# Performance work log

Hardware: AMD Instinct MI355X
Metric: run time of the kernel (lower is better)

## Reference

```python
import jax, jax.numpy as jnp
import numpy as np

GATE_THRESH = 0.4
ALPHA_FN = lambda L: 1.0 - 1.0 / L  # length-adaptive alpha, called with actual L
EPS_NORM = 1e-12  # F.normalize eps
EPS_LN = 1e-5     # LayerNorm eps


def setup_inputs() -> dict:
    key = jax.random.key(0)
    B, L, H, V = 64, 2048, 128, 32000
    ks = jax.random.split(key, 8)
    s = lambda k, shape, fan: jax.random.normal(k, shape, jnp.float32) * (1.0 / np.sqrt(fan))
    return {
        "seq": jax.random.randint(ks[0], (B, L), 0, V, dtype=jnp.int64),
        "embed_w": jax.random.normal(ks[1], (V, H), jnp.float32) * 0.02,
        "ff_w1": s(ks[2], (2 * H, H), H), "ff_b1": jnp.zeros((2 * H,), jnp.float32),
        "ff_w2": s(ks[3], (H, 2 * H), 2 * H), "ff_b2": jnp.zeros((H,), jnp.float32),
        "ln_g": jnp.ones((H,), jnp.float32), "ln_b": jnp.zeros((H,), jnp.float32),
        "kp_w": s(ks[4], (H, H), H),
        "rp_w": s(ks[5], (H, H), H), "rp_b": jnp.zeros((H,), jnp.float32),
        "out_w": s(ks[6], (V, H), H), "out_b": jnpp if False else jnp.zeros((V,), jnp.float32),
    }


def reference(seq, embed_w, ff_w1, ff_b1, ff_w2, ff_b2, ln_g, ln_b, kp_w, rp_w, rp_b, out_w, out_b):
    h = embed_w[seq]                                            # [B,L,H]
    ff = jnp.maximum(h @ ff_w1.T + ff_b1, 0.0) @ ff_w2.T + ff_b2
    x = h + ff
    mu = x.mean(-1, keepdims=True)
    var = x.var(-1, keepdims=True)                              # biased, as LayerNorm
    h = (x - mu) / jnp.sqrt(var + EPS_LN) * ln_g + ln_b
    B, L, H = h.shape
    alpha = ALPHA_FN(L)
    k_all = jnp.einsum('blh,oh->blo', h, kp_w)                  # kp has no bias

    def step(M, k):                                             # M:[B,H,H], k:[B,H]
        kn = k / jnp.maximum(jnp.linalg.norm(k, axis=-1, keepdims=True), EPS_NORM)
        vp = jnp.einsum('bij,bj->bi', M, kn)
        d = k - vp
        delta = d[:, :, None] * kn[:, None, :]                  # outer product [B,H,H]
        fire = (jnp.linalg.norm(d, axis=-1) >= GATE_THRESH * jnp.linalg.norm(k, axis=-1)).astype(k.dtype)
        return M + (1.0 - alpha) * fire[:, None, None] * delta, None

    M0 = jnp.zeros((B, H, H), h.dtype)
    M, _ = jax.lax.scan(step, M0, jnp.swapaxes(k_all[:, :-1, :], 0, 1))  # scan over L-1 steps
    q = k_all[:, -1, :]
    read = jnp.einsum('bij,bj->bi', M, q)
    return (read @ rp_w.T + rp_b) @ out_w.T + out_b             # [B,V]
```

## Files before the change

kernel.cpp:

```cpp
#include <hip/hip_runtime.h>
#include <hip/hip_bf16.h>
#include <stdint.h>

#define Bn 64
#define Ln 2048
#define Hn 128
#define Vn 32000
#define THn 256
#define LAMBDA_ (1.0f/2048.0f)
#define CC 32
#define NCH (Ln/CC)
#define KP  132
#define VS  132
#define VPW (CC*VS)
#define ADS 131
#define ADW (CC*ADS+4)
#define GS  36
#define GXS 33
#define MSR 36
#define MSW 576
#define HS  132

typedef short bf16x8 __attribute__((ext_vector_type(8)));
typedef float f32x4  __attribute__((ext_vector_type(4)));

__device__ __forceinline__ float rdlane(float v, int s) {
  return __int_as_float(__builtin_amdgcn_readlane(__float_as_int(v), s));
}

template <int CTRL>
__device__ __forceinline__ float dpp_add(float x) {
  int t = __builtin_amdgcn_update_dpp(0, __float_as_int(x), CTRL, 0xf, 0xf, false);
  return x + __int_as_float(t);
}
__device__ __forceinline__ float wave_sum64(float x) {
  x = dpp_add<0x111>(x);
  x = dpp_add<0x112>(x);
  x = dpp_add<0x114>(x);
  x = dpp_add<0x118>(x);
  x = dpp_add<0x142>(x);
  x = dpp_add<0x143>(x);
  return rdlane(x, 63);
}

__device__ __forceinline__ uint32_t packhl(float x) {
  uint32_t bx = __float_as_uint(x);
  float hf = __uint_as_float(bx & 0xFFFF0000u);
  uint32_t bl = __float_as_uint(x - hf);
  return (bx >> 16) | (bl & 0xFFFF0000u);
}
__device__ __forceinline__ float unpackhl(uint32_t u) {
  return __uint_as_float(u << 16) + __uint_as_float(u & 0xFFFF0000u);
}

struct FragHL { bf16x8 h; bf16x8 l; };
__device__ __forceinline__ FragHL mkfrag(const uint32_t* u) {
  union { uint32_t a[4]; bf16x8 v; } H, L;
  H.a[0] = __builtin_amdgcn_perm(u[1], u[0], 0x05040100u);
  H.a[1] = __builtin_amdgcn_perm(u[3], u[2], 0x05040100u);
  H.a[2] = __builtin_amdgcn_perm(u[5], u[4], 0x05040100u);
  H.a[3] = __builtin_amdgcn_perm(u[7], u[6], 0x05040100u);
  L.a[0] = __builtin_amdgcn_perm(u[1], u[0], 0x07060302u);
  L.a[1] = __builtin_amdgcn_perm(u[3], u[2], 0x07060302u);
  L.a[2] = __builtin_amdgcn_perm(u[5], u[4], 0x07060302u);
  L.a[3] = __builtin_amdgcn_perm(u[7], u[6], 0x07060302u);
  FragHL f; f.h = H.v; f.l = L.v; return f;
}

__device__ __forceinline__ void ld8(const uint32_t* p, uint32_t* u) {
  const uint4 a = *reinterpret_cast<const uint4*>(p);
  const uint4 b = *reinterpret_cast<const uint4*>(p + 4);
  u[0]=a.x; u[1]=a.y; u[2]=a.z; u[3]=a.w;
  u[4]=b.x; u[5]=b.y; u[6]=b.z; u[7]=b.w;
}

__device__ __forceinline__ bf16x8 asbf(uint4 u) {
  union { uint4 a; bf16x8 v; } c; c.a = u; return c.v;
}

__device__ __forceinline__ f32x4 mfma16(bf16x8 a, bf16x8 b, f32x4 c) {
  return __builtin_amdgcn_mfma_f32_16x16x32_bf16(a, b, c, 0, 0, 0);
}

__device__ __forceinline__ void gload_lds4(const uint32_t* g, uint32_t* l) {
  __builtin_amdgcn_global_load_lds(
      (const __attribute__((address_space(1))) void*)g,
      (__attribute__((address_space(3))) void*)l, 4, 0, 0);
}

__global__ __launch_bounds__(256) void p0_pack(
    const float* __restrict__ w1, const float* __restrict__ w2,
    const float* __restrict__ kp, uint32_t* __restrict__ wp)
{
  const int id = blockIdx.x*256 + threadIdx.x;
  const float* src; uint32_t *dh, *dl; int p;
  if (id < 16384)      { src = w1; p = id;         dh = wp;         dl = wp+16384; }
  else if (id < 32768) { src = w2; p = id-16384;   dh = wp+32768;   dl = wp+49152; }
  else                 { src = kp; p = id-32768;   dh = wp+65536;   dl = wp+73728; }
  const float x0 = src[2*p], x1 = src[2*p+1];
  const uint32_t b0 = __float_as_uint(x0), b1 = __float_as_uint(x1);
  const float l0f = x0 - __uint_as_float(b0 & 0xFFFF0000u);
  const float l1f = x1 - __uint_as_float(b1 & 0xFFFF0000u);
  dh[p] = (b0 >> 16) | ((b1 >> 16) << 16);
  dl[p] = (__float_as_uint(l0f) >> 16) | ((__float_as_uint(l1f) >> 16) << 16);
}

__global__ __launch_bounds__(256, 2) void p1_fused(
    const int* __restrict__ seq,
    const float* __restrict__ embed_w,
    const uint32_t* __restrict__ wp,
    const float* __restrict__ ff_b1, const float* __restrict__ ff_b2,
    const float* __restrict__ ln_g, const float* __restrict__ ln_b,
    uint32_t* __restrict__ knp_all, float* __restrict__ norm_all)
{
  __shared__ __align__(16) uint32_t h_p[64*HS];
  __shared__ __align__(16) uint32_t u_p[64*HS];
  __shared__ float part1[256], part2[256];
  __shared__ float mul[64], rsl[64];
  __shared__ int sid[64];

  const int tid  = threadIdx.x;
  const int lane = tid & 63;
  const int w    = __builtin_amdgcn_readfirstlane(tid >> 6);
  const int q4   = lane >> 4;
  const int m16  = lane & 15;
  const int tile0 = blockIdx.x * 64;

  const uint32_t* w1h = wp;
  const uint32_t* w1l = wp + 16384;
  const uint32_t* w2h = wp + 32768;
  const uint32_t* w2l = wp + 49152;
  const uint32_t* kph = wp + 65536;
  const uint32_t* kpl = wp + 73728;

  if (tid < 64) sid[tid] = seq[tile0 + tid];
  __syncthreads();

  {
    const int t = tid >> 2, part = tid & 3;
    const float4* erow =
        reinterpret_cast<const float4*>(embed_w + (size_t)sid[t]*Hn) + part*8;
    #pragma unroll
    for (int c = 0; c < 8; ++c) {
      float4 v = erow[c];
      int j = part*32 + c*4;
      h_p[t*HS+j+0] = packhl(v.x); h_p[t*HS+j+1] = packhl(v.y);
      h_p[t*HS+j+2] = packhl(v.z); h_p[t*HS+j+3] = packhl(v.w);
    }
  }
  __syncthreads();

  f32x4 acc2[4][2];
  #pragma unroll
  for (int tt=0;tt<4;++tt)
    #pragma unroll
    for (int ct=0;ct<2;++ct) acc2[tt][ct] = (f32x4){0.f,0.f,0.f,0.f};

  #pragma unroll 1
  for (int ho=0; ho<2; ++ho) {
    #pragma unroll 1
    for (int tt=0; tt<4; ++tt) {
      FragHL fa[4];
      #pragma unroll
      for (int kk=0;kk<4;++kk) {
        uint32_t ua[8];
        ld8(&h_p[(16*tt+m16)*HS + 32*kk + 8*q4], ua);
        fa[kk] = mkfrag(ua);
      }
      #pragma unroll
      for (int ct=0; ct<2; ++ct) {
        const int ob = 128*ho + 32*w + 16*ct;
        f32x4 a = (f32x4){0.f,0.f,0.f,0.f};
        #pragma unroll
        for (int kk=0;kk<4;++kk) {
          const size_t wi = (size_t)(ob+m16)*64 + 16*kk + 4*q4;
          bf16x8 bh = asbf(*reinterpret_cast<const uint4*>(&w1h[wi]));
          bf16x8 bl = asbf(*reinterpret_cast<const uint4*>(&w1l[wi]));
          a = mfma16(fa[kk].h, bh, a);
          a = mfma16(fa[kk].h, bl, a);
          a = mfma16(fa[kk].l, bh, a);
        }
        const float bb = ff_b1[ob + m16];
        #pragma unroll
        for (int reg=0;reg<4;++reg) {
          float uv = fmaxf(a[reg] + bb, 0.f);
          u_p[(16*tt+4*q4+reg)*HS + 32*w + 16*ct + m16] = packhl(uv);
        }
      }
    }
    __syncthreads();
    #pragma unroll 1
    for (int tt=0; tt<4; ++tt) {
      FragHL fu[4];
      #pragma unroll
      for (int kk=0;kk<4;++kk) {
        uint32_t ua[8];
        ld8(&u_p[(16*tt+m16)*HS + 32*kk + 8*q4], ua);
        fu[kk] = mkfrag(ua);
      }
      #pragma unroll
      for (int ct=0; ct<2; ++ct) {
        const int ib = 32*w + 16*ct;
        f32x4 a = acc2[tt][ct];
        #pragma unroll
        for (int kk=0;kk<4;++kk) {
          const size_t wi = (size_t)(ib+m16)*128 + 64*ho + 16*kk + 4*q4;
          bf16x8 bh = asbf(*reinterpret_cast<const uint4*>(&w2h[wi]));
          bf16x8 bl = asbf(*reinterpret_cast<const uint4*>(&w2l[wi]));
          a = mfma16(fu[kk].h, bh, a);
          a = mfma16(fu[kk].h, bl, a);
          a = mfma16(fu[kk].l, bh, a);
        }
        acc2[tt][ct] = a;
      }
    }
    __syncthreads();
  }

  float xx[4][2][4];
  #pragma unroll
  for (int tt=0;tt<4;++tt)
    #pragma unroll
    for (int ct=0;ct<2;++ct) {
      const int col = 32*w + 16*ct + m16;
      const float b2 = ff_b2[col];
      #pragma unroll
      for (int reg=0;reg<4;++reg) {
        const float hval = unpackhl(h_p[(16*tt+4*q4+reg)*HS + col]);
        xx[tt][ct][reg] = acc2[tt][ct][reg] + b2 + hval;
      }
    }
  #pragma unroll
  for (int tt=0;tt<4;++tt)
    #pragma unroll
    for (int reg=0;reg<4;++reg) {
      float s1 = xx[tt][0][reg] + xx[tt][1][reg];
      float s2 = xx[tt][0][reg]*xx[tt][0][reg] + xx[tt][1][reg]*xx[tt][1][reg];
      s1 += __shfl_xor(s1,1); s1 += __shfl_xor(s1,2);
      s1 += __shfl_xor(s1,4); s1 += __shfl_xor(s1,8);
      s2 += __shfl_xor(s2,1); s2 += __shfl_xor(s2,2);
      s2 += __shfl_xor(s2,4); s2 += __shfl_xor(s2,8);
      if (m16==0) {
        part1[w*64 + 16*tt+4*q4+reg] = s1;
        part2[w*64 + 16*tt+4*q4+reg] = s2;
      }
    }
  __syncthreads();
  if (tid < 64) {
    const float mu = (part1[tid]+part1[64+tid]+part1[128+tid]+part1[192+tid])*(1.0f/128.0f);
    const float ms = (part2[tid]+part2[64+tid]+part2[128+tid]+part2[192+tid])*(1.0f/128.0f);
    mul[tid] = mu;
    rsl[tid] = rsqrtf(ms - mu*mu + 1e-5f);
  }
  __syncthreads();

  #pragma unroll
  for (int tt=0;tt<4;++tt)
    #pragma unroll
    for (int ct=0;ct<2;++ct) {
      const int col = 32*w + 16*ct + m16;
      const float g = ln_g[col], bb = ln_b[col];
      #pragma unroll
      for (int reg=0;reg<4;++reg) {
        const int tok = 16*tt+4*q4+reg;
        const float hn = (xx[tt][ct][reg] - mul[tok])*rsl[tok]*g + bb;
        h_p[tok*HS + col] = packhl(hn);
      }
    }
  __syncthreads();

  f32x4 ak[4][2];
  #pragma unroll 1
  for (int tt=0;tt<4;++tt) {
    FragHL fh[4];
    #pragma unroll
    for (int kk=0;kk<4;++kk) {
      uint32_t ua[8];
      ld8(&h_p[(16*tt+m16)*HS + 32*kk + 8*q4], ua);
      fh[kk] = mkfrag(ua);
    }
    #pragma unroll
    for (int ct=0;ct<2;++ct) {
      const int ob = 32*w + 16*ct;
      f32x4 a = (f32x4){0.f,0.f,0.f,0.f};
      #pragma unroll
      for (int kk=0;kk<4;++kk) {
        const size_t wi = (size_t)(ob+m16)*64 + 16*kk + 4*q4;
        bf16x8 bh = asbf(*reinterpret_cast<const uint4*>(&kph[wi]));
        bf16x8 bl = asbf(*reinterpret_cast<const uint4*>(&kpl[wi]));
        a = mfma16(fh[kk].h, bh, a);
        a = mfma16(fh[kk].h, bl, a);
        a = mfma16(fh[kk].l, bh, a);
      }
      ak[tt][ct] = a;
    }
  }
  #pragma unroll
  for (int tt=0;tt<4;++tt)
    #pragma unroll
    for (int reg=0;reg<4;++reg) {
      float s = ak[tt][0][reg]*ak[tt][0][reg] + ak[tt][1][reg]*ak[tt][1][reg];
      s += __shfl_xor(s,1); s += __shfl_xor(s,2);
      s += __shfl_xor(s,4); s += __shfl_xor(s,8);
      if (m16==0) part1[w*64 + 16*tt+4*q4+reg] = s;
    }
  __syncthreads();
  if (tid < 64) {
    const float nn = part1[tid]+part1[64+tid]+part1[128+tid]+part1[192+tid];
    const float nrm = sqrtf(nn);
    norm_all[tile0 + tid] = nrm;
    mul[tid] = 1.0f / fmaxf(nrm, 1e-12f);
  }
  __syncthreads();
  #pragma unroll
  for (int tt=0;tt<4;++tt)
    #pragma unroll
    for (int ct=0;ct<2;++ct) {
      const int col = 32*w + 16*ct + m16;
      #pragma unroll
      for (int reg=0;reg<4;++reg) {
        const int tok = 16*tt+4*q4+reg;
        knp_all[(size_t)(tile0+tok)*Hn + col] = packhl(ak[tt][ct][reg]*mul[tok]);
      }
    }
}

__global__ __launch_bounds__(576, 1) void p2_scan(
    const uint32_t* __restrict__ knp_all, const float* __restrict__ norm_all,
    float* __restrict__ read_ws)
{
  const int tid  = threadIdx.x;
  const int lane = tid & 63;
  const int wv   = __builtin_amdgcn_readfirstlane(tid >> 6);
  const int q    = lane >> 4;
  const int m    = lane & 15;
  const int b    = blockIdx.x;

  __shared__ __align__(16) uint32_t kn_p[3*CC*KP];
  __shared__ __align__(16) float    vp0L[2*VPW];
  __shared__ __align__(16) float    adL [2*ADW];
  __shared__ __align__(16) float    Gt  [2*CC*GS];
  __shared__ __align__(16) float    GxT [CC*GXS];
  __shared__ __align__(16) uint32_t msc [8*MSW];
  __shared__ float nrm_l[3*CC];

  f32x4 Macc[8];
  #pragma unroll
  for (int ct=0; ct<8; ++ct) Macc[ct] = (f32x4){0.f,0.f,0.f,0.f};

  const uint32_t* knb = knp_all + (size_t)b*Ln*Hn;
  const float*    nb  = norm_all + (size_t)b*Ln;

  const int swm  = ((m>>3)&3)<<3;
  const int swm2 = (((16+m)>>3)&3)<<3;

  {
    if (tid < 256) {
      const int t = tid>>3, g = tid&7;
      const int sw = ((t>>3)&3)<<3;
      const uint4* src = reinterpret_cast<const uint4*>(knb + t*Hn + g*16);
      uint32_t* dstb = &kn_p[t*KP];
      *reinterpret_cast<uint4*>(&dstb[(16*g+0) ^ sw])  = src[0];
      *reinterpret_cast<uint4*>(&dstb[(16*g+4) ^ sw])  = src[1];
      *reinterpret_cast<uint4*>(&dstb[(16*g+8) ^ sw])  = src[2];
      *reinterpret_cast<uint4*>(&dstb[(16*g+12) ^ sw]) = src[3];
    } else if (tid < 512) {
      const int idx = tid-256, t = idx>>3, g = idx&7;
      const int sw = ((t>>3)&3)<<3;
      const uint4* src = reinterpret_cast<const uint4*>(knb + CC*Hn + t*Hn + g*16);
      uint32_t* dstb = &kn_p[CC*KP + t*KP];
      *reinterpret_cast<uint4*>(&dstb[(16*g+0) ^ sw])  = src[0];
      *reinterpret_cast<uint4*>(&dstb[(16*g+4) ^ sw])  = src[1];
      *reinterpret_cast<uint4*>(&dstb[(16*g+8) ^ sw])  = src[2];
      *reinterpret_cast<uint4*>(&dstb[(16*g+12) ^ sw]) = src[3];
    } else {
      nrm_l[tid-512] = nb[tid-512];
    }
  }
  __syncthreads();

  {
    if (wv >= 5) {
      const int ti = (wv-5)>>1, si = (wv-5)&1;
      const int ra = 16*ti+m, rb = 16*si+m;
      const int swa = ((ra>>3)&3)<<3, swb = ((rb>>3)&3)<<3;
      f32x4 g4 = (f32x4){0.f,0.f,0.f,0.f};
      #pragma unroll
      for (int kk=0; kk<4; ++kk) {
        uint32_t ua[8], ub[8];
        ld8(&kn_p[ra*KP + ((32*kk + 8*q) ^ swa)], ua);
        ld8(&kn_p[rb*KP + ((32*kk + 8*q) ^ swb)], ub);
        FragHL fa = mkfrag(ua), fb = mkfrag(ub);
        g4 = mfma16(fa.h, fb.h, g4);
        g4 = mfma16(fa.h, fb.l, g4);
        g4 = mfma16(fa.l, fb.h, g4);
      }
      #pragma unroll
      for (int reg=0; reg<4; ++reg)
        Gt[(16*ti + 4*q + reg)*GS + 16*si + m] = g4[reg];
    }
    if (wv >= 1) {
      const int h0 = 16*(wv-1);
      const float nr0 = nrm_l[m], nr1 = nrm_l[16+m];
      const uint4 r0 = *reinterpret_cast<const uint4*>(&kn_p[m*KP + ((h0 + 4*q) ^ swm)]);
      const uint4 r1 = *reinterpret_cast<const uint4*>(&kn_p[(16+m)*KP + ((h0 + 4*q) ^ swm2)]);
      const uint32_t* pr0 = &r0.x; const uint32_t* pr1 = &r1.x;
      #pragma unroll
      for (int reg=0; reg<4; ++reg) {
        const int h = h0 + 4*q + reg;
        vp0L[m*VS + h]      = nr0*unpackhl(pr0[reg]);
        vp0L[(16+m)*VS + h] = nr1*unpackhl(pr1[reg]);
      }
    }
  }
  __syncthreads();

  #pragma unroll 1
  for (int ch=0; ch<NCH; ++ch) {
    const int cur = ch%3, nx1 = (ch+1)%3, nx2 = (ch+2)%3;
    const int sel = ch & 1;
    const uint32_t* knc = &kn_p[cur*CC*KP];
    const uint32_t* knN = &kn_p[nx1*CC*KP];
    const uint32_t* knP = &kn_p[nx2*CC*KP];
    const bool havn  = (ch+1 < NCH);
    const bool havn2 = (ch+2 < NCH);

    float pfn = 0.f;
    if (havn2 && tid >= 288 && tid < 320) pfn = nb[(ch+2)*CC + (tid-288)];

    if (wv==0) {
      float ad0[CC], ad1[CC], gr[CC];
      float* adW = &adL[sel*ADW];
      const float* vpR = &vp0L[sel*VPW];
      const float* GtS = &Gt[sel*CC*GS];
      #pragma unroll
      for (int t=0;t<CC;++t) gr[t] = GtS[t*GS + (lane&31)];
      const float nrmv = nrm_l[cur*CC + (lane&31)];
      #pragma unroll
      for (int t=0;t<CC;++t) {
        float a0c0 = vpR[t*VS + lane];
        float a1c0 = vpR[t*VS + 64 + lane];
        float a0c1=0.f, a0c2=0.f, a0c3=0.f;
        float a1c1=0.f, a1c2=0.f, a1c3=0.f;
        #pragma unroll
        for (int s=0; s<t; ++s) {
          const float g = rdlane(gr[t], s);
          switch (s & 3) {
            case 0: a0c0 -= g*ad0[s]; a1c0 -= g*ad1[s]; break;
            case 1: a0c1 -= g*ad0[s]; a1c1 -= g*ad1[s]; break;
            case 2: a0c2 -= g*ad0[s]; a1c2 -= g*ad1[s]; break;
            default:a0c3 -= g*ad0[s]; a1c3 -= g*ad1[s]; break;
          }
        }
        const float acc0 = (a0c0+a0c1)+(a0c2+a0c3);
        const float acc1 = (a1c0+a1c1)+(a1c2+a1c3);
        const float sqt = wave_sum64(acc0*acc0 + acc1*acc1);
        const float nrm = rdlane(nrmv, t);
        if (ch==NCH-1 && t==CC-1) {
          const int swt = ((t>>3)&3)<<3;
          const float kn0 = unpackhl(knc[t*KP + (lane ^ swt)]);
          const float kn1 = unpackhl(knc[t*KP + ((64+lane) ^ swt)]);
          read_ws[b*Hn + lane]      = nrm*(nrm*kn0 - acc0);
          read_ws[b*Hn + 64 + lane] = nrm*(nrm*kn1 - acc1);
        } else {
          const float at = (sqt >= 0.16f*nrm*nrm) ? LAMBDA_ : 0.f;
          ad0[t] = at*acc0; ad1[t] = at*acc1;
          adW[t*ADS + lane]      = ad0[t];
          adW[t*ADS + 64 + lane] = ad1[t];
        }
      }
    } else if (havn) {
      const int h0 = 16*(wv-1);
      if (ch >= 1) {
        const float* adR = &adL[(1-sel)*ADW];
        uint32_t ap[8];
        #pragma unroll
        for (int j=0;j<8;++j)
          ap[j] = packhl(adR[(8*q+j)*ADS + h0 + m]);
        FragHL fa = mkfrag(ap);
        #pragma unroll
        for (int ct=0; ct<8; ++ct) {
          uint32_t bu[8];
          #pragma unroll
          for (int j=0;j<8;++j)
            bu[j] = knP[(8*q+j)*KP + ((16*ct+m) ^ (q<<3))];
          FragHL fb = mkfrag(bu);
          Macc[ct] = mfma16(fa.h, fb.h, Macc[ct]);
          Macc[ct] = mfma16(fa.h, fb.l, Macc[ct]);
          Macc[ct] = mfma16(fa.l, fb.h, Macc[ct]);
        }
      }
      {
        f32x4 v0 = (f32x4){0.f,0.f,0.f,0.f};
        f32x4 v1 = (f32x4){0.f,0.f,0.f,0.f};
        uint32_t* mybase = &msc[(wv-1)*MSW];
        #pragma unroll
        for (int kk=0; kk<4; ++kk) {
          #pragma unroll
          for (int c2=0; c2<2; ++c2) {
            const int ct = 2*kk + c2;
            #pragma unroll
            for (int reg=0; reg<4; ++reg)
              mybase[(4*q+reg)*MSR + 16*c2 + m] = packhl(Macc[ct][reg]);
          }
          uint32_t ua[8], ub[8];
          ld8(&mybase[m*MSR + 8*q], ua);
          FragHL fa = mkfrag(ua);
          ld8(&knN[m*KP + ((32*kk + 8*q) ^ swm)], ub);
          FragHL fb = mkfrag(ub);
          v0 = mfma16(fa.h, fb.h, v0);
          v0 = mfma16(fa.h, fb.l, v0);
          v0 = mfma16(fa.l, fb.h, v0);
          ld8(&knN[(16+m)*KP + ((32*kk + 8*q) ^ swm2)], ub);
          fb = mkfrag(ub);
          v1 = mfma16(fa.h, fb.h, v1);
          v1 = mfma16(fa.h, fb.l, v1);
          v1 = mfma16(fa.l, fb.h, v1);
        }
        float* vpW = &vp0L[(1-sel)*VPW];
        const float nr0 = nrm_l[nx1*CC + m];
        const float nr1 = nrm_l[nx1*CC + 16 + m];
        const uint4 r0 = *reinterpret_cast<const uint4*>(&knN[m*KP + ((h0 + 4*q) ^ swm)]);
        const uint4 r1 = *reinterpret_cast<const uint4*>(&knN[(16+m)*KP + ((h0 + 4*q) ^ swm2)]);
        const uint32_t* pr0 = &r0.x; const uint32_t* pr1 = &r1.x;
        #pragma unroll
        for (int reg=0; reg<4; ++reg) {
          const int h = h0 + 4*q + reg;
          vpW[m*VS + h]      = nr0*unpackhl(pr0[reg]) - v0[reg];
          vpW[(16+m)*VS + h] = nr1*unpackhl(pr1[reg]) - v1[reg];
        }
      }
      if (wv <= 4) {
        const int tj = (wv-1)>>1, ts = (wv-1)&1;
        const int ra = 16*tj+m, rb = 16*ts+m;
        const int swa = ((ra>>3)&3)<<3, swb = ((rb>>3)&3)<<3;
        f32x4 g4 = (f32x4){0.f,0.f,0.f,0.f};
        #pragma unroll
        for (int kk=0; kk<4; ++kk) {
          uint32_t ua[8], ub[8];
          ld8(&knN[ra*KP + ((32*kk + 8*q) ^ swa)], ua);
          ld8(&knc[rb*KP + ((32*kk + 8*q) ^ swb)], ub);
          FragHL fa = mkfrag(ua), fb = mkfrag(ub);
          g4 = mfma16(fa.h, fb.h, g4);
          g4 = mfma16(fa.h, fb.l, g4);
          g4 = mfma16(fa.l, fb.h, g4);
        }
        #pragma unroll
        for (int reg=0; reg<4; ++reg)
          GxT[(16*tj + 4*q + reg)*GXS + 16*ts + m] = g4[reg];
      } else {
        const int ti = (wv-5)>>1, si = (wv-5)&1;
        const int ra = 16*ti+m, rb = 16*si+m;
        const int swa = ((ra>>3)&3)<<3, swb = ((rb>>3)&3)<<3;
        f32x4 g4 = (f32x4){0.f,0.f,0.f,0.f};
        #pragma unroll
        for (int kk=0; kk<4; ++kk) {
          uint32_t ua[8], ub[8];
          ld8(&knN[ra*KP + ((32*kk + 8*q) ^ swa)], ua);
          ld8(&knN[rb*KP + ((32*kk + 8*q) ^ swb)], ub);
          FragHL fa = mkfrag(ua), fb = mkfrag(ub);
          g4 = mfma16(fa.h, fb.h, g4);
          g4 = mfma16(fa.h, fb.l, g4);
          g4 = mfma16(fa.l, fb.h, g4);
        }
        #pragma unroll
        for (int reg=0; reg<4; ++reg)
          Gt[(1-sel)*CC*GS + (16*ti + 4*q + reg)*GS + 16*si + m] = g4[reg];
      }
    }
    __syncthreads();
    if (ch==NCH-1) break;

    if (wv >= 1) {
      const int h0 = 16*(wv-1);
      f32x4 c0 = (f32x4){0.f,0.f,0.f,0.f};
      f32x4 c1 = (f32x4){0.f,0.f,0.f,0.f};
      {
        const float* adR = &adL[sel*ADW];
        uint32_t* mybase = &msc[(wv-1)*MSW];
        #pragma unroll
        for (int c2=0; c2<2; ++c2)
          #pragma unroll
          for (int reg=0; reg<4; ++reg)
            mybase[(4*q+reg)*MSR + 16*c2 + m] =
                packhl(adR[(16*c2+m)*ADS + h0 + 4*q + reg]);
        uint32_t ua[8], gb[8];
        ld8(&mybase[m*MSR + 8*q], ua);
        FragHL fa = mkfrag(ua);
        #pragma unroll
        for (int jj=0;jj<8;++jj) gb[jj] = packhl(GxT[m*GXS + 8*q + jj]);
        FragHL fb = mkfrag(gb);
        c0 = mfma16(fa.h, fb.h, c0);
        c0 = mfma16(fa.h, fb.l, c0);
        c0 = mfma16(fa.l, fb.h, c0);
        #pragma unroll
        for (int jj=0;jj<8;++jj) gb[jj] = packhl(GxT[(16+m)*GXS + 8*q + jj]);
        fb = mkfrag(gb);
        c1 = mfma16(fa.h, fb.h, c1);
        c1 = mfma16(fa.h, fb.l, c1);
        c1 = mfma16(fa.l, fb.h, c1);
      }
      {
        float* vpW = &vp0L[(1-sel)*VPW];
        #pragma unroll
        for (int reg=0; reg<4; ++reg) {
          const int h = h0 + 4*q + reg;
          vpW[m*VS + h]      -= c0[reg];
          vpW[(16+m)*VS + h] -= c1[reg];
        }
      }
      if (havn2) {
        const uint32_t* gsrc = knb + (size_t)(ch+2)*CC*Hn;
        uint32_t* ldst = &kn_p[nx2*CC*KP];
        #pragma unroll
        for (int r=0; r<4; ++r) {
          const int t = (wv-1)*4 + r;
          const int sw = ((t>>3)&3)<<3;
          #pragma unroll
          for (int half=0; half<2; ++half) {
            gload_lds4(gsrc + t*Hn + ((half*64 + lane) ^ sw),
                       &ldst[t*KP + half*64]);
          }
        }
        if (tid >= 288 && tid < 320) nrm_l[nx2*CC + (tid-288)] = pfn;
      }
    }
    __syncthreads();
  }
}

__global__ __launch_bounds__(128) void p3a(
    const float* __restrict__ read_ws, const float* __restrict__ rp_w,
    const float* __restrict__ rp_b, float* __restrict__ o1_ws)
{
  __shared__ float rd[128];
  const int b = blockIdx.x, t = threadIdx.x;
  rd[t] = read_ws[b*Hn + t];
  __syncthreads();
  float acc = rp_b[t];
  const float* wr = rp_w + t*Hn;
  #pragma unroll 4
  for (int i = 0; i < Hn; ++i) acc += rd[i]*wr[i];
  o1_ws[b*Hn + t] = acc;
}

__global__ __launch_bounds__(256) void p3b(
    const float* __restrict__ o1_ws, const float* __restrict__ out_w,
    const float* __restrict__ out_b, float* __restrict__ out)
{
  __shared__ __align__(16) float o1[8192];
  const int tid = threadIdx.x;
  #pragma unroll
  for (int c = 0; c < 32; ++c) o1[c*256+tid] = o1_ws[c*256+tid];
  __syncthreads();
  const int v = blockIdx.x*256 + tid;
  float acc[64];
  const float ob = out_b[v];
  #pragma unroll
  for (int bb = 0; bb < 64; ++bb) acc[bb] = ob;
  const float4* wrow = reinterpret_cast<const float4*>(out_w + (size_t)v*Hn);
  #pragma unroll 1
  for (int r4 = 0; r4 < 32; ++r4) {
    const float4 wv = wrow[r4];
    #pragma unroll
    for (int bb = 0; bb < 64; ++bb) {
      const float4 ov = *reinterpret_cast<const float4*>(&o1[bb*Hn + r4*4]);
      acc[bb] += wv.x*ov.x + wv.y*ov.y + wv.z*ov.z + wv.w*ov.w;
    }
  }
  #pragma unroll
  for (int bb = 0; bb < 64; ++bb) out[(size_t)bb*Vn + v] = acc[bb];
}

extern "C" void kernel_launch(void* const* d_in, const int* in_sizes, int n_in,
                              void* d_out, int out_size, void* d_ws, size_t ws_size,
                              hipStream_t stream)
{
  const int*   seq     = (const int*)  d_in[0];
  const float* embed_w = (const float*)d_in[1];
  const float* ff_w1   = (const float*)d_in[2];
  const float* ff_b1   = (const float*)d_in[3];
  const float* ff_w2   = (const float*)d_in[4];
  const float* ff_b2   = (const float*)d_in[5];
  const float* ln_g    = (const float*)d_in[6];
  const float* ln_b    = (const float*)d_in[7];
  const float* kp_w    = (const float*)d_in[8];
  const float* rp_w    = (const float*)d_in[9];
  const float* rp_b    = (const float*)d_in[10];
  const float* out_w   = (const float*)d_in[11];
  const float* out_b   = (const float*)d_in[12];

  float* ws          = (float*)d_ws;
  uint32_t* knp_all  = (uint32_t*)ws;
  float* norm_all    = ws + (size_t)Bn*Ln*Hn;
  float* read_ws     = norm_all + (size_t)Bn*Ln;
  float* o1_ws       = read_ws + Bn*Hn;
  uint32_t* wp       = (uint32_t*)(o1_ws + Bn*Hn);

  p0_pack<<<dim3(160), dim3(256), 0, stream>>>(ff_w1, ff_w2, kp_w, wp);
  p1_fused<<<dim3(2048), dim3(256), 0, stream>>>(
      seq, embed_w, wp, ff_b1, ff_b2, ln_g, ln_b, knp_all, norm_all);
  p2_scan<<<dim3(64), dim3(576), 0, stream>>>(knp_all, norm_all, read_ws);
  p3a<<<dim3(64), dim3(128), 0, stream>>>(read_ws, rp_w, rp_b, o1_ws);
  p3b<<<dim3(125), dim3(256), 0, stream>>>(o1_ws, out_w, out_b, (float*)d_out);
}
```

Before: 800.7 us.

## Split scan block into dedicated wave groups and prefetch Gram rows in serial wave

The scan kernel grows from 9 to 16 waves. Eight waves handle the M update and value projection, four compute the cross-chunk Gram tile, and three compute the symmetric intra-chunk Gram, mirroring the off-diagonal block instead of computing it twice. The serial wave 0 now streams Gram rows from LDS with a two-row prefetch instead of holding all 32 in registers, and runs at raised scheduling priority. The aim is to take the Gram work off the critical path of the M-update waves and relieve register pressure in the serial solve, at the cost of more waves competing for the CU.

```diff
diff --git a/kernel.cpp b/kernel.cpp
--- a/kernel.cpp
+++ b/kernel.cpp
@@ -325,7 +325,7 @@
     }
 }
 
-__global__ __launch_bounds__(576, 1) void p2_scan(
+__global__ __launch_bounds__(1024, 1) void p2_scan(
     const uint32_t* __restrict__ knp_all, const float* __restrict__ norm_all,
     float* __restrict__ read_ws)
 {
@@ -373,15 +373,17 @@
       *reinterpret_cast<uint4*>(&dstb[(16*g+4) ^ sw])  = src[1];
       *reinterpret_cast<uint4*>(&dstb[(16*g+8) ^ sw])  = src[2];
       *reinterpret_cast<uint4*>(&dstb[(16*g+12) ^ sw]) = src[3];
-    } else {
+    } else if (tid < 512+2*CC) {
       nrm_l[tid-512] = nb[tid-512];
     }
   }
   __syncthreads();
 
   {
-    if (wv >= 5) {
-      const int ti = (wv-5)>>1, si = (wv-5)&1;
+    if (wv >= 13) {
+      const int gi = wv - 13;
+      const int ti = (gi==2) ? 1 : 0;
+      const int si = (gi==0) ? 0 : 1;
       const int ra = 16*ti+m, rb = 16*si+m;
       const int swa = ((ra>>3)&3)<<3, swb = ((rb>>3)&3)<<3;
       f32x4 g4 = (f32x4){0.f,0.f,0.f,0.f};
@@ -398,8 +400,13 @@
       #pragma unroll
       for (int reg=0; reg<4; ++reg)
         Gt[(16*ti + 4*q + reg)*GS + 16*si + m] = g4[reg];
-    }
-    if (wv >= 1) {
+      if (gi==1) {
+        #pragma unroll
+        for (int reg=0; reg<4; ++reg)
+          Gt[(16*si + m)*GS + 16*ti + 4*q + reg] = g4[reg];
+      }
+    }
+    if (wv >= 1 && wv <= 8) {
       const int h0 = 16*(wv-1);
       const float nr0 = nrm_l[m], nr1 = nrm_l[16+m];
       const uint4 r0 = *reinterpret_cast<const uint4*>(&kn_p[m*KP + ((h0 + 4*q) ^ swm)]);
@@ -429,22 +436,26 @@
     if (havn2 && tid >= 288 && tid < 320) pfn = nb[(ch+2)*CC + (tid-288)];
 
     if (wv==0) {
-      float ad0[CC], ad1[CC], gr[CC];
+      float ad0[CC], ad1[CC];
       float* adW = &adL[sel*ADW];
       const float* vpR = &vp0L[sel*VPW];
       const float* GtS = &Gt[sel*CC*GS];
-      #pragma unroll
-      for (int t=0;t<CC;++t) gr[t] = GtS[t*GS + (lane&31)];
-      const float nrmv = nrm_l[cur*CC + (lane&31)];
+      const int lid = lane & 31;
+      const float nrmv = nrm_l[cur*CC + lid];
+      float grt = GtS[0*GS + lid];
+      float grn = GtS[1*GS + lid];
+      __builtin_amdgcn_s_setprio(1);
       #pragma unroll
       for (int t=0;t<CC;++t) {
+        float grn2 = 0.f;
+        if (t+2 < CC) grn2 = GtS[(t+2)*GS + lid];
         float a0c0 = vpR[t*VS + lane];
         float a1c0 = vpR[t*VS + 64 + lane];
         float a0c1=0.f, a0c2=0.f, a0c3=0.f;
         float a1c1=0.f, a1c2=0.f, a1c3=0.f;
         #pragma unroll
         for (int s=0; s<t; ++s) {
-          const float g = rdlane(gr[t], s);
+          const float g = rdlane(grt, s);
           switch (s & 3) {
             case 0: a0c0 -= g*ad0[s]; a1c0 -= g*ad1[s]; break;
             case 1: a0c1 -= g*ad0[s]; a1c1 -= g*ad1[s]; break;
@@ -468,70 +479,75 @@
           adW[t*ADS + lane]      = ad0[t];
           adW[t*ADS + 64 + lane] = ad1[t];
         }
-      }
-    } else if (havn) {
-      const int h0 = 16*(wv-1);
-      if (ch >= 1) {
-        const float* adR = &adL[(1-sel)*ADW];
-        uint32_t ap[8];
-        #pragma unroll
-        for (int j=0;j<8;++j)
-          ap[j] = packhl(adR[(8*q+j)*ADS + h0 + m]);
-        FragHL fa = mkfrag(ap);
-        #pragma unroll
-        for (int ct=0; ct<8; ++ct) {
-          uint32_t bu[8];
+        grt = grn; grn = grn2;
+      }
+      __builtin_amdgcn_s_setprio(0);
+    } else if (wv <= 8) {
+      if (havn) {
+        const int h0 = 16*(wv-1);
+        if (ch >= 1) {
+          const float* adR = &adL[(1-sel)*ADW];
+          uint32_t ap[8];
           #pragma unroll
           for (int j=0;j<8;++j)
-            bu[j] = knP[(8*q+j)*KP + ((16*ct+m) ^ (q<<3))];
-          FragHL fb = mkfrag(bu);
-          Macc[ct] = mfma16(fa.h, fb.h, Macc[ct]);
-          Macc[ct] = mfma16(fa.h, fb.l, Macc[ct]);
-          Macc[ct] = mfma16(fa.l, fb.h, Macc[ct]);
-        }
-      }
-      {
-        f32x4 v0 = (f32x4){0.f,0.f,0.f,0.f};
-        f32x4 v1 = (f32x4){0.f,0.f,0.f,0.f};
-        uint32_t* mybase = &msc[(wv-1)*MSW];
-        #pragma unroll
-        for (int kk=0; kk<4; ++kk) {
+            ap[j] = packhl(adR[(8*q+j)*ADS + h0 + m]);
+          FragHL fa = mkfrag(ap);
           #pragma unroll
-          for (int c2=0; c2<2; ++c2) {
-            const int ct = 2*kk + c2;
+          for (int ct=0; ct<8; ++ct) {
+            uint32_t bu[8];
             #pragma unroll
-            for (int reg=0; reg<4; ++reg)
-              mybase[(4*q+reg)*MSR + 16*c2 + m] = packhl(Macc[ct][reg]);
+            for (int j=0;j<8;++j)
+              bu[j] = knP[(8*q+j)*KP + ((16*ct+m) ^ (q<<3))];
+            FragHL fb = mkfrag(bu);
+            Macc[ct] = mfma16(fa.h, fb.h, Macc[ct]);
+            Macc[ct] = mfma16(fa.h, fb.l, Macc[ct]);
+            Macc[ct] = mfma16(fa.l, fb.h, Macc[ct]);
           }
-          uint32_t ua[8], ub[8];
-          ld8(&mybase[m*MSR + 8*q], ua);
-          FragHL fa = mkfrag(ua);
-          ld8(&knN[m*KP + ((32*kk + 8*q) ^ swm)], ub);
-          FragHL fb = mkfrag(ub);
-          v0 = mfma16(fa.h, fb.h, v0);
-          v0 = mfma16(fa.h, fb.l, v0);
-          v0 = mfma16(fa.l, fb.h, v0);
-          ld8(&knN[(16+m)*KP + ((32*kk + 8*q) ^ swm2)], ub);
-          fb = mkfrag(ub);
-          v1 = mfma16(fa.h, fb.h, v1);
-          v1 = mfma16(fa.h, fb.l, v1);
-          v1 = mfma16(fa.l, fb.h, v1);
-        }
-        float* vpW = &vp0L[(1-sel)*VPW];
-        const float nr0 = nrm_l[nx1*CC + m];
-        const float nr1 = nrm_l[nx1*CC + 16 + m];
-        const uint4 r0 = *reinterpret_cast<const uint4*>(&knN[m*KP + ((h0 + 4*q) ^ swm)]);
-        const uint4 r1 = *reinterpret_cast<const uint4*>(&knN[(16+m)*KP + ((h0 + 4*q) ^ swm2)]);
-        const uint32_t* pr0 = &r0.x; const uint32_t* pr1 = &r1.x;
-        #pragma unroll
-        for (int reg=0; reg<4; ++reg) {
-          const int h = h0 + 4*q + reg;
-          vpW[m*VS + h]      = nr0*unpackhl(pr0[reg]) - v0[reg];
-          vpW[(16+m)*VS + h] = nr1*unpackhl(pr1[reg]) - v1[reg];
-        }
-      }
-      if (wv <= 4) {
-        const int tj = (wv-1)>>1, ts = (wv-1)&1;
+        }
+        {
+          f32x4 v0 = (f32x4){0.f,0.f,0.f,0.f};
+          f32x4 v1 = (f32x4){0.f,0.f,0.f,0.f};
+          uint32_t* mybase = &msc[(wv-1)*MSW];
+          #pragma unroll
+          for (int kk=0; kk<4; ++kk) {
+            #pragma unroll
+            for (int c2=0; c2<2; ++c2) {
+              const int ct = 2*kk + c2;
+              #pragma unroll
+              for (int reg=0; reg<4; ++reg)
+                mybase[(4*q+reg)*MSR + 16*c2 + m] = packhl(Macc[ct][reg]);
+            }
+            uint32_t ua[8], ub[8];
+            ld8(&mybase[m*MSR + 8*q], ua);
+            FragHL fa = mkfrag(ua);
+            ld8(&knN[m*KP + ((32*kk + 8*q) ^ swm)], ub);
+            FragHL fb = mkfrag(ub);
+            v0 = mfma16(fa.h, fb.h, v0);
+            v0 = mfma16(fa.h, fb.l, v0);
+            v0 = mfma16(fa.l, fb.h, v0);
+            ld8(&knN[(16+m)*KP + ((32*kk + 8*q) ^ swm2)], ub);
+            fb = mkfrag(ub);
+            v1 = mfma16(fa.h, fb.h, v1);
+            v1 = mfma16(fa.h, fb.l, v1);
+            v1 = mfma16(fa.l, fb.h, v1);
+          }
+          float* vpW = &vp0L[(1-sel)*VPW];
+          const float nr0 = nrm_l[nx1*CC + m];
+          const float nr1 = nrm_l[nx1*CC + 16 + m];
+          const uint4 r0 = *reinterpret_cast<const uint4*>(&knN[m*KP + ((h0 + 4*q) ^ swm)]);
+          const uint4 r1 = *reinterpret_cast<const uint4*>(&knN[(16+m)*KP + ((h0 + 4*q) ^ swm2)]);
+          const uint32_t* pr0 = &r0.x; const uint32_t* pr1 = &r1.x;
+          #pragma unroll
+          for (int reg=0; reg<4; ++reg) {
+            const int h = h0 + 4*q + reg;
+            vpW[m*VS + h]      = nr0*unpackhl(pr0[reg]) - v0[reg];
+            vpW[(16+m)*VS + h] = nr1*unpackhl(pr1[reg]) - v1[reg];
+          }
+        }
+      }
+    } else if (wv <= 12) {
+      if (havn) {
+        const int tj = (wv-9)>>1, ts = (wv-9)&1;
         const int ra = 16*tj+m, rb = 16*ts+m;
         const int swa = ((ra>>3)&3)<<3, swb = ((rb>>3)&3)<<3;
         f32x4 g4 = (f32x4){0.f,0.f,0.f,0.f};
@@ -548,8 +564,12 @@
         #pragma unroll
         for (int reg=0; reg<4; ++reg)
           GxT[(16*tj + 4*q + reg)*GXS + 16*ts + m] = g4[reg];
-      } else {
-        const int ti = (wv-5)>>1, si = (wv-5)&1;
+      }
+    } else {
+      if (havn) {
+        const int gi = wv - 13;
+        const int ti = (gi==2) ? 1 : 0;
+        const int si = (gi==0) ? 0 : 1;
         const int ra = 16*ti+m, rb = 16*si+m;
         const int swa = ((ra>>3)&3)<<3, swb = ((rb>>3)&3)<<3;
         f32x4 g4 = (f32x4){0.f,0.f,0.f,0.f};
@@ -563,15 +583,21 @@
           g4 = mfma16(fa.h, fb.l, g4);
           g4 = mfma16(fa.l, fb.h, g4);
         }
+        float* GtW = &Gt[(1-sel)*CC*GS];
         #pragma unroll
         for (int reg=0; reg<4; ++reg)
-          Gt[(1-sel)*CC*GS + (16*ti + 4*q + reg)*GS + 16*si + m] = g4[reg];
+          GtW[(16*ti + 4*q + reg)*GS + 16*si + m] = g4[reg];
+        if (gi==1) {
+          #pragma unroll
+          for (int reg=0; reg<4; ++reg)
+            GtW[(16*si + m)*GS + 16*ti + 4*q + reg] = g4[reg];
+        }
       }
     }
     __syncthreads();
     if (ch==NCH-1) break;
 
-    if (wv >= 1) {
+    if (wv >= 1 && wv <= 8) {
       const int h0 = 16*(wv-1);
       f32x4 c0 = (f32x4){0.f,0.f,0.f,0.f};
       f32x4 c1 = (f32x4){0.f,0.f,0.f,0.f};
@@ -700,7 +726,7 @@
   p0_pack<<<dim3(160), dim3(256), 0, stream>>>(ff_w1, ff_w2, kp_w, wp);
   p1_fused<<<dim3(2048), dim3(256), 0, stream>>>(
       seq, embed_w, wp, ff_b1, ff_b2, ln_g, ln_b, knp_all, norm_all);
-  p2_scan<<<dim3(64), dim3(576), 0, stream>>>(knp_all, norm_all, read_ws);
+  p2_scan<<<dim3(64), dim3(1024), 0, stream>>>(knp_all, norm_all, read_ws);
   p3a<<<dim3(64), dim3(128), 0, stream>>>(read_ws, rp_w, rp_b, o1_ws);
   p3b<<<dim3(125), dim3(256), 0, stream>>>(o1_ws, out_w, out_b, (float*)d_out);
 }
```

Measured after the change: 792.5 us. No clear change (-1.0%).
